# Performance work log

Hardware: AMD Instinct MI355X
Metric: run time of the kernel (lower is better)

The kernel has to match this reference:

```python
import jax, jax.numpy as jnp
import numpy as np

HIDDEN = 512
HEADS = 8
HEAD_DIM = HIDDEN // HEADS   # 64
MAN_DIM = 256                # manifold_dim = hidden_dim // 2
SCALE = HEAD_DIM ** -0.5


def _c(re, im):
    return jax.lax.complex(re, im)


def setup_inputs() -> dict:
    key = jax.random.key(0)
    ks = jax.random.split(key, 13)
    def w(k, shape, fan_in):
        return (jax.random.normal(k, shape, dtype=jnp.float32) / np.sqrt(fan_in)).astype(jnp.float32)
    B, S = 2, 2048
    return {
        "x": jax.random.normal(ks[0], (B, S, HIDDEN), dtype=jnp.float32),
        "Wq_re": w(ks[1], (HIDDEN, HIDDEN), HIDDEN), "Wq_im": w(ks[2], (HIDDEN, HIDDEN), HIDDEN),
        "Wk_re": w(ks[3], (HIDDEN, HIDDEN), HIDDEN), "Wk_im": w(ks[4], (HIDDEN, HIDDEN), HIDDEN),
        "Wv_re": w(ks[5], (HIDDEN, HIDDEN), HIDDEN), "Wv_im": w(ks[6], (HIDDEN, HIDDEN), HIDDEN),
        "Wm_re": w(ks[7], (HEAD_DIM, MAN_DIM), HEAD_DIM), "Wm_im": w(ks[8], (HEAD_DIM, MAN_DIM), HEAD_DIM),
        "Wmi_re": w(ks[9], (MAN_DIM, HEAD_DIM), MAN_DIM), "Wmi_im": w(ks[10], (MAN_DIM, HEAD_DIM), MAN_DIM),
        "Wo_re": w(ks[11], (HIDDEN, HIDDEN), HIDDEN), "Wo_im": w(ks[12], (HIDDEN, HIDDEN), HIDDEN),
    }


def reference(x, Wq_re, Wq_im, Wk_re, Wk_im, Wv_re, Wv_im,
              Wm_re, Wm_im, Wmi_re, Wmi_im, Wo_re, Wo_im):
    B, S, D = x.shape
    # quantum state preparation: cast to complex, L2-normalize along last dim
    xc = x.astype(jnp.complex64)
    norm = jnp.linalg.norm(xc, axis=-1, keepdims=True)
    xc = xc / norm

    Wq, Wk, Wv = _c(Wq_re, Wq_im), _c(Wk_re, Wk_im), _c(Wv_re, Wv_im)
    Wm, Wmi, Wo = _c(Wm_re, Wm_im), _c(Wmi_re, Wmi_im), _c(Wo_re, Wo_im)

    def heads(t):  # [B,S,D] -> [B,H,S,head_dim]
        return t.reshape(B, S, HEADS, HEAD_DIM).transpose(0, 2, 1, 3)

    q = heads(xc @ Wq)
    k = heads(xc @ Wk)
    v = heads(xc @ Wv)

    # project each head onto the manifold (complex linear)
    qm = jnp.einsum('bhsd,dm->bhsm', q, Wm)
    km = jnp.einsum('bhsd,dm->bhsm', k, Wm)
    vm = jnp.einsum('bhsd,dm->bhsm', v, Wm)

    # Hermitian inner product attention scores; softmax over real part
    scores = jnp.einsum('bhqm,bhkm->bhqk', qm, jnp.conj(km)) * SCALE
    attn = jax.nn.softmax(scores.real, axis=-1).astype(jnp.complex64)

    outm = jnp.einsum('bhqk,bhkm->bhqm', attn, vm)
    out = jnp.einsum('bhsm,md->bhsd', outm, Wmi)        # back to head_dim
    out = out.transpose(0, 2, 1, 3).reshape(B, S, D)    # merge heads
    out = out @ Wo
    # return real/imag stacked as float32 (complex64 output -> [B,S,D,2])
    return jnp.stack([out.real, out.imag], axis=-1)
```

## Files before the change

kernel.cpp:

```cpp
#include <hip/hip_runtime.h>
#include <hip/hip_bf16.h>
#include <stdint.h>


typedef __attribute__((ext_vector_type(8))) short bf16x8;
typedef __attribute__((ext_vector_type(4))) float f32x4;

#define QSCALE 0.18033688011112042f

__device__ __forceinline__ unsigned short f2b(float f) {
    union { float f; unsigned int u; } v; v.f = f;
    unsigned int r = v.u + 0x7fffu + ((v.u >> 16) & 1u);
    return (unsigned short)(r >> 16);
}

__device__ __forceinline__ unsigned int cvtpk(float a, float b) {
    union { __hip_bfloat162 h; unsigned int u; } v;
    v.h = __float22bfloat162_rn(make_float2(a, b));
    return v.u;
}

__device__ __forceinline__ void ld16(void* lds, const void* g) {
    __builtin_amdgcn_global_load_lds(
        (__attribute__((address_space(1))) unsigned int*)(g),
        (__attribute__((address_space(3))) unsigned int*)(lds), 16, 0, 0);
}

__global__ __launch_bounds__(256) void k_prep(
        const float* __restrict__ x, unsigned short* __restrict__ xn,
        const float* __restrict__ s0, const float* __restrict__ s1,
        const float* __restrict__ s2, const float* __restrict__ s3,
        const float* __restrict__ s4, const float* __restrict__ s5,
        const float* __restrict__ s6, const float* __restrict__ s7,
        float* __restrict__ d0, float* __restrict__ d1,
        float* __restrict__ d2, float* __restrict__ d3,
        float* __restrict__ d4, float* __restrict__ d5,
        float* __restrict__ d6, float* __restrict__ d7) {
    __shared__ float tile[64][65];
    if (blockIdx.x < 1024) {
        int row  = blockIdx.x * 4 + (threadIdx.x >> 6);
        int lane = threadIdx.x & 63;
        const float4* xr = (const float4*)(x + (size_t)row * 512);
        float4 a = xr[lane], b = xr[lane + 64];
        float s = a.x*a.x + a.y*a.y + a.z*a.z + a.w*a.w
                + b.x*b.x + b.y*b.y + b.z*b.z + b.w*b.w;
        #pragma unroll
        for (int m = 1; m < 64; m <<= 1) s += __shfl_xor(s, m, 64);
        float inv = 1.0f / sqrtf(s);
        ushort4 o;
        o.x = f2b(a.x*inv); o.y = f2b(a.y*inv); o.z = f2b(a.z*inv); o.w = f2b(a.w*inv);
        *(ushort4*)&xn[(size_t)row*512 + lane*4] = o;
        o.x = f2b(b.x*inv); o.y = f2b(b.y*inv); o.z = f2b(b.z*inv); o.w = f2b(b.w*inv);
        *(ushort4*)&xn[(size_t)row*512 + 256 + lane*4] = o;
        return;
    }
    int bid = blockIdx.x - 1024;
    const float* src; float* dst; int R, C, tr, tc;
    if (bid < 384) {
        int mat = bid >> 6, tl = bid & 63;
        src = (mat==0)?s0:(mat==1)?s1:(mat==2)?s2:(mat==3)?s3:(mat==4)?s4:s5;
        dst = (mat==0)?d0:(mat==1)?d1:(mat==2)?d2:(mat==3)?d3:(mat==4)?d4:d5;
        R = 512; C = 512; tr = tl >> 3; tc = tl & 7;
    } else {
        int mat = (bid - 384) >> 2, tl = (bid - 384) & 3;
        src = mat ? s7 : s6; dst = mat ? d7 : d6;
        R = 64; C = 256; tr = 0; tc = tl;
    }
    int r0 = tr * 64, c0 = tc * 64;
    int tx = threadIdx.x & 63, ty = threadIdx.x >> 6;
    #pragma unroll
    for (int i = 0; i < 16; i++) {
        int r = ty + i*4;
        tile[r][tx] = src[(size_t)(r0 + r)*C + c0 + tx];
    }
    __syncthreads();
    #pragma unroll
    for (int i = 0; i < 16; i++) {
        int r = ty + i*4;
        dst[(size_t)(c0 + r)*R + r0 + tx] = tile[tx][r];
    }
}

__global__ __launch_bounds__(256) void k_gh(const float* __restrict__ Wm_re, const float* __restrict__ Wm_im,
                                            const float* __restrict__ WmT_re, const float* __restrict__ WmT_im,
                                            const float* __restrict__ Wmi_re, const float* __restrict__ Wmi_im,
                                            float* __restrict__ GH) {
    int id = blockIdx.x * 256 + threadIdx.x;
    int mat = id >> 12;
    int a = (id >> 6) & 63, c = id & 63;
    float s = 0.f;
    if (mat < 2) {
        for (int m = 0; m < 256; m++) {
            float ar = Wm_re[a*256+m], ai = Wm_im[a*256+m];
            float br = WmT_re[m*64+c], bi = WmT_im[m*64+c];
            s += (mat == 0) ? (ar*br + ai*bi) : (ai*br - ar*bi);
        }
        GH[id] = s;
    } else {
        for (int m = 0; m < 256; m++) {
            float ar = Wm_re[a*256+m], ai = Wm_im[a*256+m];
            float br = Wmi_re[m*64+c], bi = Wmi_im[m*64+c];
            s += (mat == 2) ? (ar*br - ai*bi) : (ar*bi + ai*br);
        }
        GH[mat*4096 + c*64 + a] = s;
    }
}

__global__ __launch_bounds__(256) void k_pack(
        const float* __restrict__ WqT_re, const float* __restrict__ WqT_im,
        const float* __restrict__ WkT_re, const float* __restrict__ WkT_im,
        const float* __restrict__ WvT_re, const float* __restrict__ WvT_im,
        const float* __restrict__ Wo_re,  const float* __restrict__ Wo_im,
        const float* __restrict__ GH,
        unsigned short* __restrict__ WqkvT, unsigned short* __restrict__ Wbig) {
    if (blockIdx.x < 6144) {
        int id = blockIdx.x * 256 + threadIdx.x;
        int n = id >> 9, k = id & 511;
        float val;
        if (n < 1024) {
            int h = n >> 7, part = (n >> 6) & 1, j = n & 63;
            const float* Gr = GH;
            const float* Gi = GH + 4096;
            const float* qr = WqT_re + (size_t)(h*64)*512 + k;
            const float* qi = WqT_im + (size_t)(h*64)*512 + k;
            float s = 0.f;
            if (part == 0) { for (int d = 0; d < 64; d++) s += qr[d*512]*Gr[d*64+j] - qi[d*512]*Gi[d*64+j]; }
            else           { for (int d = 0; d < 64; d++) s += qr[d*512]*Gi[d*64+j] + qi[d*512]*Gr[d*64+j]; }
            val = s * QSCALE;
        } else if (n < 2048) {
            int m = n - 1024; int h = m >> 7, part = (m >> 6) & 1, j = m & 63;
            val = (part ? WkT_im : WkT_re)[(size_t)(h*64+j)*512 + k];
        } else {
            int m = n - 2048; int h = m >> 7, part = (m >> 6) & 1, j = m & 63;
            val = (part ? WvT_im : WvT_re)[(size_t)(h*64+j)*512 + k];
        }
        WqkvT[id] = f2b(val);
    } else {
        int id = (blockIdx.x - 6144) * 256 + threadIdx.x;
        int np = id >> 10, kk = id & 1023;
        int c = np >> 1, p = np & 1;
        int h = kk >> 7, pp = (kk >> 6) & 1, d = kk & 63;
        const float* HrT = GH + 2*4096;
        const float* HiT = GH + 3*4096;
        float s = 0.f;
        if (p == pp) {
            for (int j = 0; j < 64; j++) {
                float hr = HrT[j*64+d], hi = HiT[j*64+d];
                float wr = Wo_re[(size_t)(h*64+j)*512 + c];
                float wi = Wo_im[(size_t)(h*64+j)*512 + c];
                s += hr*wr - hi*wi;
            }
        } else {
            for (int j = 0; j < 64; j++) {
                float hr = HrT[j*64+d], hi = HiT[j*64+d];
                float wr = Wo_re[(size_t)(h*64+j)*512 + c];
                float wi = Wo_im[(size_t)(h*64+j)*512 + c];
                s += hr*wi + hi*wr;
            }
            if (p == 0) s = -s;
        }
        Wbig[(size_t)np*1024 + kk] = f2b(s);
    }
}

template<int MODE, int MT>
__global__ __launch_bounds__(256, 2) void k_gemm(
        const unsigned short* __restrict__ Ain, const unsigned short* __restrict__ Btin,
        void* __restrict__ Cout, unsigned short* __restrict__ Vt, int K) {
    __shared__ __align__(16) unsigned short Al[MT*32];
    __shared__ __align__(16) unsigned short Bl[128*32];
    const int t = threadIdx.x;
    const int wave = t >> 6, lane = t & 63, quad = lane >> 4, l16 = lane & 15;
    const int wr = wave >> 1, wc = wave & 1;

    const unsigned short* A;
    const unsigned short* Bt;
    unsigned short* Cb = nullptr;
    int m0, n0;
    if (MODE == 0) {
        if (blockIdx.y < 16) {
            A = Ain; Bt = Btin;
            m0 = blockIdx.x * 128; n0 = blockIdx.y * 128;
            Cb = (unsigned short*)Cout;
        } else {
            int idx = (blockIdx.y - 16) * 32 + blockIdx.x;
            int b = idx >> 7, mt = (idx >> 4) & 7, nt = idx & 15;
            A  = Btin + 2048*512;
            Bt = Ain + (size_t)b*2048*512;
            m0 = mt * 128; n0 = nt * 128;
            Cb = Vt + (size_t)b*1024*2048;
        }
    } else {
        A = Ain; Bt = Btin;
        m0 = blockIdx.x * MT; n0 = blockIdx.y * 128;
    }

    f32x4 acc[MT/32][4] = {};
    for (int kt = 0; kt < K; kt += 32) {
        #pragma unroll
        for (int i = 0; i < MT/64; i++) {
            int g = t + i*256, r = g >> 2, gr = g & 3;
            ld16(&Al[g*8], &A[(size_t)(m0 + r)*K + kt + gr*8]);
        }
        #pragma unroll
        for (int i = 0; i < 2; i++) {
            int g = t + i*256, r = g >> 2, gr = g & 3;
            ld16(&Bl[g*8], &Bt[(size_t)(n0 + r)*K + kt + gr*8]);
        }
        __syncthreads();
        bf16x8 af[MT/32], bfr[4];
        #pragma unroll
        for (int rt = 0; rt < MT/32; rt++)
            af[rt] = *(const bf16x8*)&Al[(wr*(MT/2) + rt*16 + l16)*32 + quad*8];
        #pragma unroll
        for (int ct = 0; ct < 4; ct++)
            bfr[ct] = *(const bf16x8*)&Bl[(wc*64 + ct*16 + l16)*32 + quad*8];
        #pragma unroll
        for (int rt = 0; rt < MT/32; rt++)
            #pragma unroll
            for (int ct = 0; ct < 4; ct++)
                acc[rt][ct] = __builtin_amdgcn_mfma_f32_16x16x32_bf16(af[rt], bfr[ct], acc[rt][ct], 0, 0, 0);
        __syncthreads();
    }
    #pragma unroll
    for (int rt = 0; rt < MT/32; rt++) {
        int row = m0 + wr*(MT/2) + rt*16 + quad*4;
        #pragma unroll
        for (int ct = 0; ct < 4; ct++) {
            int col = n0 + wc*64 + ct*16 + l16;
            if (MODE == 0) {
                unsigned int u01 = cvtpk(acc[rt][ct][0], acc[rt][ct][1]);
                unsigned int u23 = cvtpk(acc[rt][ct][2], acc[rt][ct][3]);
                Cb[(size_t)(row+0)*2048 + col] = (unsigned short)(u01);
                Cb[(size_t)(row+1)*2048 + col] = (unsigned short)(u01 >> 16);
                Cb[(size_t)(row+2)*2048 + col] = (unsigned short)(u23);
                Cb[(size_t)(row+3)*2048 + col] = (unsigned short)(u23 >> 16);
            } else {
                float* C = (float*)Cout;
                #pragma unroll
                for (int r = 0; r < 4; r++)
                    C[(size_t)(row + r)*1024 + col] = acc[rt][ct][r];
            }
        }
    }
}

__global__ __launch_bounds__(256, 2) void k_attn(
        const unsigned short* __restrict__ QK,
        const unsigned short* __restrict__ Vt,
        float* __restrict__ Opart,
        float* __restrict__ Lpart) {
    __shared__ __align__(16) unsigned short Kl[2][8192];
    __shared__ __align__(16) unsigned short Vl[2][8192];
    __shared__ __align__(16) unsigned short Pl[4608];

    const int t = threadIdx.x, w = t >> 6, lane = t & 63, quad = lane >> 4, l16 = lane & 15;
    const int bh = blockIdx.x, b = bh >> 3, h = bh & 7;
    const int qb = blockIdx.y & 15, half = blockIdx.y >> 4;
    const int tok0 = b*2048 + qb*128;

    bf16x8 qf[2][4];
    #pragma unroll
    for (int rt = 0; rt < 2; rt++)
        #pragma unroll
        for (int ks = 0; ks < 4; ks++)
            qf[rt][ks] = *(const bf16x8*)&QK[(size_t)(tok0 + w*32 + rt*16 + l16)*2048 + h*128 + ks*32 + quad*8];

    const unsigned short* kp = QK + (size_t)(b*2048 + half*1024 + (t >> 2))*2048 + 1024 + h*128 + (t & 3)*8;
    const unsigned short* vp = Vt + (size_t)(b*1024 + h*128 + (t >> 2))*2048 + half*1024 + (t & 3)*8;

    f32x4 Oacc[2][8] = {};
    float ls[2][4] = {};

    #pragma unroll
    for (int i = 0; i < 4; i++) ld16(&Kl[0][(i*256 + t)*8], kp + i*32);
    #pragma unroll
    for (int i = 0; i < 4; i++) ld16(&Vl[0][(i*256 + t)*8], vp + (i & 1)*131072 + (i >> 1)*32);
    __syncthreads();

    for (int it = 0; it < 16; it++) {
        const int cur = it & 1;
        if (it < 15) {
            int kt2 = (it + 1) * 64;
            #pragma unroll
            for (int i = 0; i < 4; i++) ld16(&Kl[cur^1][(i*256 + t)*8], kp + (size_t)kt2*2048 + i*32);
            #pragma unroll
            for (int i = 0; i < 4; i++) ld16(&Vl[cur^1][(i*256 + t)*8], vp + kt2 + (i & 1)*131072 + (i >> 1)*32);
        }

        f32x4 S[2][4] = {};
        #pragma unroll
        for (int ks = 0; ks < 4; ks++) {
            #pragma unroll
            for (int ct = 0; ct < 4; ct++) {
                bf16x8 kf = *(const bf16x8*)&Kl[cur][ks*2048 + (ct*16 + l16)*32 + quad*8];
                #pragma unroll
                for (int rt = 0; rt < 2; rt++)
                    S[rt][ct] = __builtin_amdgcn_mfma_f32_16x16x32_bf16(qf[rt][ks], kf, S[rt][ct], 0, 0, 0);
            }
        }
        #pragma unroll
        for (int ks2 = 0; ks2 < 2; ks2++) {
            #pragma unroll
            for (int rt = 0; rt < 2; rt++) {
                #pragma unroll
                for (int ct2 = 0; ct2 < 2; ct2++) {
                    int ct = ks2*2 + ct2;
                    float p0 = exp2f(S[rt][ct][0]), p1 = exp2f(S[rt][ct][1]);
                    float p2 = exp2f(S[rt][ct][2]), p3 = exp2f(S[rt][ct][3]);
                    ls[rt][0] += p0; ls[rt][1] += p1; ls[rt][2] += p2; ls[rt][3] += p3;
                    int q = w*32 + rt*16 + quad*4;
                    int base = ct2*16 + l16;
                    unsigned int u01 = cvtpk(p0, p1);
                    unsigned int u23 = cvtpk(p2, p3);
                    Pl[base + (q+0)*36] = (unsigned short)(u01);
                    Pl[base + (q+1)*36] = (unsigned short)(u01 >> 16);
                    Pl[base + (q+2)*36] = (unsigned short)(u23);
                    Pl[base + (q+3)*36] = (unsigned short)(u23 >> 16);
                }
            }
            bf16x8 pf[2];
            #pragma unroll
            for (int rt = 0; rt < 2; rt++)
                pf[rt] = *(const bf16x8*)&Pl[(w*32 + rt*16 + l16)*36 + quad*8];
            #pragma unroll
            for (int dt = 0; dt < 8; dt++) {
                bf16x8 vf = *(const bf16x8*)&Vl[cur][ks2*4096 + (dt*16 + l16)*32 + quad*8];
                #pragma unroll
                for (int rt = 0; rt < 2; rt++)
                    Oacc[rt][dt] = __builtin_amdgcn_mfma_f32_16x16x32_bf16(pf[rt], vf, Oacc[rt][dt], 0, 0, 0);
            }
        }
        __syncthreads();
    }

    #pragma unroll
    for (int rt = 0; rt < 2; rt++)
        #pragma unroll
        for (int r = 0; r < 4; r++) {
            float s = ls[rt][r];
            #pragma unroll
            for (int m = 1; m < 16; m <<= 1) s += __shfl_xor(s, m, 64);
            ls[rt][r] = s;
        }
    float* Op = Opart + (size_t)half*4096*1024;
    float* Lp = Lpart + (size_t)half*32768;
    #pragma unroll
    for (int rt = 0; rt < 2; rt++) {
        int q = w*32 + rt*16 + quad*4;
        int tok = tok0 + q;
        if (l16 == 0) {
            #pragma unroll
            for (int r = 0; r < 4; r++) Lp[(size_t)(tok + r)*8 + h] = ls[rt][r];
        }
        #pragma unroll
        for (int dt = 0; dt < 8; dt++) {
            int col = h*128 + dt*16 + l16;
            #pragma unroll
            for (int r = 0; r < 4; r++)
                Op[(size_t)(tok + r)*1024 + col] = Oacc[rt][dt][r];
        }
    }
}

__global__ __launch_bounds__(256) void k_merge(const float* __restrict__ Opart,
                                               const float* __restrict__ Lpart,
                                               unsigned short* __restrict__ O) {
    int tid = blockIdx.x * 256 + threadIdx.x;
    #pragma unroll
    for (int rep = 0; rep < 2; rep++) {
        int slot = tid + rep * 524288;
        int tok = slot >> 8, cg = slot & 255, h = cg >> 5;
        float l0 = Lpart[(size_t)tok*8 + h];
        float l1 = Lpart[32768 + (size_t)tok*8 + h];
        float inv = 1.0f / (l0 + l1);
        float4 a = ((const float4*)Opart)[slot];
        float4 b = ((const float4*)Opart)[1048576 + slot];
        unsigned int u01 = cvtpk((a.x + b.x)*inv, (a.y + b.y)*inv);
        unsigned int u23 = cvtpk((a.z + b.z)*inv, (a.w + b.w)*inv);
        ushort4 o;
        o.x = (unsigned short)u01; o.y = (unsigned short)(u01 >> 16);
        o.z = (unsigned short)u23; o.w = (unsigned short)(u23 >> 16);
        ((ushort4*)O)[slot] = o;
    }
}

extern "C" void kernel_launch(void* const* d_in, const int* in_sizes, int n_in,
                              void* d_out, int out_size, void* d_ws, size_t ws_size,
                              hipStream_t stream) {
    (void)in_sizes; (void)n_in; (void)out_size; (void)ws_size;
    const float* x      = (const float*)d_in[0];
    const float* Wq_re  = (const float*)d_in[1];
    const float* Wq_im  = (const float*)d_in[2];
    const float* Wk_re  = (const float*)d_in[3];
    const float* Wk_im  = (const float*)d_in[4];
    const float* Wv_re  = (const float*)d_in[5];
    const float* Wv_im  = (const float*)d_in[6];
    const float* Wm_re  = (const float*)d_in[7];
    const float* Wm_im  = (const float*)d_in[8];
    const float* Wmi_re = (const float*)d_in[9];
    const float* Wmi_im = (const float*)d_in[10];
    const float* Wo_re  = (const float*)d_in[11];
    const float* Wo_im  = (const float*)d_in[12];

    char* ws = (char*)d_ws;
    unsigned short* xn    = (unsigned short*)(ws);
    unsigned short* WqkvT = (unsigned short*)(ws + (4u << 20));
    unsigned short* Wbig  = (unsigned short*)(ws + (7u << 20));
    float*          GH    = (float*)         (ws + (9u << 20));
    float*          WmT_re= (float*)         (ws + (9u << 20) + (64u << 10));
    float*          WmT_im= (float*)         (ws + (9u << 20) + (128u << 10));
    unsigned short* QK    = (unsigned short*)(ws + (10u << 20));
    unsigned short* Vt    = (unsigned short*)(ws + (26u << 20));
    unsigned short* Obuf  = (unsigned short*)(ws + (34u << 20));
    float*          Opart = (float*)         (ws + (42u << 20));
    float*          Lpart = (float*)         (ws + (74u << 20));
    float* WqT_re = (float*)(ws + (10u << 20));
    float* WqT_im = (float*)(ws + (11u << 20));
    float* WkT_re = (float*)(ws + (12u << 20));
    float* WkT_im = (float*)(ws + (13u << 20));
    float* WvT_re = (float*)(ws + (14u << 20));
    float* WvT_im = (float*)(ws + (15u << 20));

    k_prep      <<<dim3(1416), dim3(256), 0, stream>>>(
        x, xn,
        Wq_re, Wq_im, Wk_re, Wk_im, Wv_re, Wv_im, Wm_re, Wm_im,
        WqT_re, WqT_im, WkT_re, WkT_im, WvT_re, WvT_im, WmT_re, WmT_im);
    k_gh        <<<dim3(64),   dim3(256), 0, stream>>>(Wm_re, Wm_im, WmT_re, WmT_im, Wmi_re, Wmi_im, GH);
    k_pack      <<<dim3(10240),dim3(256), 0, stream>>>(
        WqT_re, WqT_im, WkT_re, WkT_im, WvT_re, WvT_im, Wo_re, Wo_im, GH, WqkvT, Wbig);
    k_gemm<0,128><<<dim3(32, 24), dim3(256), 0, stream>>>(xn, WqkvT, (void*)QK, Vt, 512);
    k_attn      <<<dim3(16, 32), dim3(256), 0, stream>>>(QK, Vt, Opart, Lpart);
    k_merge     <<<dim3(2048), dim3(256), 0, stream>>>(Opart, Lpart, Obuf);
    k_gemm<1,64> <<<dim3(64, 8), dim3(256), 0, stream>>>(Obuf, Wbig, d_out, nullptr, 1024);
}
```

Measured before the change: 253.5 us.

## Split attention keys four ways with bf16 normalized partials and smaller tiles

The attention kernel now splits the key range into four quarters instead of two, doubling the grid to 1024 blocks. It uses 32-key tiles, so LDS per block is halved, and occupancy is raised to 3 blocks per CU. Each split normalizes its own output and stores it as bf16 rather than fp32, which cuts partial-buffer traffic. The merge kernel reads four bf16 partials and combines them with softmax-sum weights using vectorized loads. The trade-offs are extra bf16 rounding in the partials and more per-tile sync overhead.

```diff
diff --git a/kernel.cpp b/kernel.cpp
--- a/kernel.cpp
+++ b/kernel.cpp
@@ -12,6 +12,12 @@
     union { float f; unsigned int u; } v; v.f = f;
     unsigned int r = v.u + 0x7fffu + ((v.u >> 16) & 1u);
     return (unsigned short)(r >> 16);
+}
+
+__device__ __forceinline__ float b2f(short s) {
+    union { float f; unsigned int u; } v;
+    v.u = ((unsigned int)(unsigned short)s) << 16;
+    return v.f;
 }
 
 __device__ __forceinline__ unsigned int cvtpk(float a, float b) {
@@ -245,19 +251,20 @@
     }
 }
 
-__global__ __launch_bounds__(256, 2) void k_attn(
+__global__ __launch_bounds__(256, 3) void k_attn(
         const unsigned short* __restrict__ QK,
         const unsigned short* __restrict__ Vt,
-        float* __restrict__ Opart,
+        unsigned short* __restrict__ Opart,
         float* __restrict__ Lpart) {
-    __shared__ __align__(16) unsigned short Kl[2][8192];
-    __shared__ __align__(16) unsigned short Vl[2][8192];
+    __shared__ __align__(16) unsigned short Kl[2][4096];
+    __shared__ __align__(16) unsigned short Vl[2][4096];
     __shared__ __align__(16) unsigned short Pl[4608];
 
     const int t = threadIdx.x, w = t >> 6, lane = t & 63, quad = lane >> 4, l16 = lane & 15;
     const int bh = blockIdx.x, b = bh >> 3, h = bh & 7;
-    const int qb = blockIdx.y & 15, half = blockIdx.y >> 4;
+    const int qb = blockIdx.y >> 2, quarter = blockIdx.y & 3;
     const int tok0 = b*2048 + qb*128;
+    const int key0 = quarter*512;
 
     bf16x8 qf[2][4];
     #pragma unroll
@@ -266,70 +273,67 @@
         for (int ks = 0; ks < 4; ks++)
             qf[rt][ks] = *(const bf16x8*)&QK[(size_t)(tok0 + w*32 + rt*16 + l16)*2048 + h*128 + ks*32 + quad*8];
 
-    const unsigned short* kp = QK + (size_t)(b*2048 + half*1024 + (t >> 2))*2048 + 1024 + h*128 + (t & 3)*8;
-    const unsigned short* vp = Vt + (size_t)(b*1024 + h*128 + (t >> 2))*2048 + half*1024 + (t & 3)*8;
+    const unsigned short* kp = QK + (size_t)(b*2048 + key0 + ((t >> 2) & 31))*2048 + 1024 + h*128
+                               + (t >> 7)*32 + (t & 3)*8;
+    const unsigned short* vp = Vt + (size_t)(b*1024 + h*128 + (t >> 2))*2048 + key0 + (t & 3)*8;
 
     f32x4 Oacc[2][8] = {};
     float ls[2][4] = {};
 
     #pragma unroll
-    for (int i = 0; i < 4; i++) ld16(&Kl[0][(i*256 + t)*8], kp + i*32);
-    #pragma unroll
-    for (int i = 0; i < 4; i++) ld16(&Vl[0][(i*256 + t)*8], vp + (i & 1)*131072 + (i >> 1)*32);
+    for (int i = 0; i < 2; i++) ld16(&Kl[0][(i*256 + t)*8], kp + i*64);
+    #pragma unroll
+    for (int i = 0; i < 2; i++) ld16(&Vl[0][(i*256 + t)*8], vp + (size_t)i*64*2048);
     __syncthreads();
 
     for (int it = 0; it < 16; it++) {
         const int cur = it & 1;
         if (it < 15) {
-            int kt2 = (it + 1) * 64;
-            #pragma unroll
-            for (int i = 0; i < 4; i++) ld16(&Kl[cur^1][(i*256 + t)*8], kp + (size_t)kt2*2048 + i*32);
-            #pragma unroll
-            for (int i = 0; i < 4; i++) ld16(&Vl[cur^1][(i*256 + t)*8], vp + kt2 + (i & 1)*131072 + (i >> 1)*32);
-        }
-
-        f32x4 S[2][4] = {};
+            int kt2 = (it + 1) * 32;
+            #pragma unroll
+            for (int i = 0; i < 2; i++) ld16(&Kl[cur^1][(i*256 + t)*8], kp + (size_t)kt2*2048 + i*64);
+            #pragma unroll
+            for (int i = 0; i < 2; i++) ld16(&Vl[cur^1][(i*256 + t)*8], vp + kt2 + (size_t)i*64*2048);
+        }
+
+        f32x4 S[2][2] = {};
         #pragma unroll
         for (int ks = 0; ks < 4; ks++) {
             #pragma unroll
-            for (int ct = 0; ct < 4; ct++) {
-                bf16x8 kf = *(const bf16x8*)&Kl[cur][ks*2048 + (ct*16 + l16)*32 + quad*8];
+            for (int ct = 0; ct < 2; ct++) {
+                bf16x8 kf = *(const bf16x8*)&Kl[cur][ks*1024 + (ct*16 + l16)*32 + quad*8];
                 #pragma unroll
                 for (int rt = 0; rt < 2; rt++)
                     S[rt][ct] = __builtin_amdgcn_mfma_f32_16x16x32_bf16(qf[rt][ks], kf, S[rt][ct], 0, 0, 0);
             }
         }
         #pragma unroll
-        for (int ks2 = 0; ks2 < 2; ks2++) {
-            #pragma unroll
-            for (int rt = 0; rt < 2; rt++) {
-                #pragma unroll
-                for (int ct2 = 0; ct2 < 2; ct2++) {
-                    int ct = ks2*2 + ct2;
-                    float p0 = exp2f(S[rt][ct][0]), p1 = exp2f(S[rt][ct][1]);
-                    float p2 = exp2f(S[rt][ct][2]), p3 = exp2f(S[rt][ct][3]);
-                    ls[rt][0] += p0; ls[rt][1] += p1; ls[rt][2] += p2; ls[rt][3] += p3;
-                    int q = w*32 + rt*16 + quad*4;
-                    int base = ct2*16 + l16;
-                    unsigned int u01 = cvtpk(p0, p1);
-                    unsigned int u23 = cvtpk(p2, p3);
-                    Pl[base + (q+0)*36] = (unsigned short)(u01);
-                    Pl[base + (q+1)*36] = (unsigned short)(u01 >> 16);
-                    Pl[base + (q+2)*36] = (unsigned short)(u23);
-                    Pl[base + (q+3)*36] = (unsigned short)(u23 >> 16);
-                }
+        for (int rt = 0; rt < 2; rt++) {
+            #pragma unroll
+            for (int ct = 0; ct < 2; ct++) {
+                float p0 = exp2f(S[rt][ct][0]), p1 = exp2f(S[rt][ct][1]);
+                float p2 = exp2f(S[rt][ct][2]), p3 = exp2f(S[rt][ct][3]);
+                ls[rt][0] += p0; ls[rt][1] += p1; ls[rt][2] += p2; ls[rt][3] += p3;
+                int q = w*32 + rt*16 + quad*4;
+                int base = ct*16 + l16;
+                unsigned int u01 = cvtpk(p0, p1);
+                unsigned int u23 = cvtpk(p2, p3);
+                Pl[base + (q+0)*36] = (unsigned short)(u01);
+                Pl[base + (q+1)*36] = (unsigned short)(u01 >> 16);
+                Pl[base + (q+2)*36] = (unsigned short)(u23);
+                Pl[base + (q+3)*36] = (unsigned short)(u23 >> 16);
             }
-            bf16x8 pf[2];
+        }
+        bf16x8 pf[2];
+        #pragma unroll
+        for (int rt = 0; rt < 2; rt++)
+            pf[rt] = *(const bf16x8*)&Pl[(w*32 + rt*16 + l16)*36 + quad*8];
+        #pragma unroll
+        for (int dt = 0; dt < 8; dt++) {
+            bf16x8 vf = *(const bf16x8*)&Vl[cur][(dt*16 + l16)*32 + quad*8];
             #pragma unroll
             for (int rt = 0; rt < 2; rt++)
-                pf[rt] = *(const bf16x8*)&Pl[(w*32 + rt*16 + l16)*36 + quad*8];
-            #pragma unroll
-            for (int dt = 0; dt < 8; dt++) {
-                bf16x8 vf = *(const bf16x8*)&Vl[cur][ks2*4096 + (dt*16 + l16)*32 + quad*8];
-                #pragma unroll
-                for (int rt = 0; rt < 2; rt++)
-                    Oacc[rt][dt] = __builtin_amdgcn_mfma_f32_16x16x32_bf16(pf[rt], vf, Oacc[rt][dt], 0, 0, 0);
-            }
+                Oacc[rt][dt] = __builtin_amdgcn_mfma_f32_16x16x32_bf16(pf[rt], vf, Oacc[rt][dt], 0, 0, 0);
         }
         __syncthreads();
     }
@@ -343,12 +347,15 @@
             for (int m = 1; m < 16; m <<= 1) s += __shfl_xor(s, m, 64);
             ls[rt][r] = s;
         }
-    float* Op = Opart + (size_t)half*4096*1024;
-    float* Lp = Lpart + (size_t)half*32768;
+    unsigned short* Op = Opart + (size_t)quarter*4096*1024;
+    float* Lp = Lpart + (size_t)quarter*32768;
     #pragma unroll
     for (int rt = 0; rt < 2; rt++) {
         int q = w*32 + rt*16 + quad*4;
         int tok = tok0 + q;
+        float inv[4];
+        #pragma unroll
+        for (int r = 0; r < 4; r++) inv[r] = 1.0f / ls[rt][r];
         if (l16 == 0) {
             #pragma unroll
             for (int r = 0; r < 4; r++) Lp[(size_t)(tok + r)*8 + h] = ls[rt][r];
@@ -358,31 +365,35 @@
             int col = h*128 + dt*16 + l16;
             #pragma unroll
             for (int r = 0; r < 4; r++)
-                Op[(size_t)(tok + r)*1024 + col] = Oacc[rt][dt][r];
-        }
-    }
-}
-
-__global__ __launch_bounds__(256) void k_merge(const float* __restrict__ Opart,
+                Op[(size_t)(tok + r)*1024 + col] = f2b(Oacc[rt][dt][r] * inv[r]);
+        }
+    }
+}
+
+__global__ __launch_bounds__(256) void k_merge(const unsigned short* __restrict__ Opart,
                                                const float* __restrict__ Lpart,
                                                unsigned short* __restrict__ O) {
-    int tid = blockIdx.x * 256 + threadIdx.x;
-    #pragma unroll
-    for (int rep = 0; rep < 2; rep++) {
-        int slot = tid + rep * 524288;
-        int tok = slot >> 8, cg = slot & 255, h = cg >> 5;
-        float l0 = Lpart[(size_t)tok*8 + h];
-        float l1 = Lpart[32768 + (size_t)tok*8 + h];
-        float inv = 1.0f / (l0 + l1);
-        float4 a = ((const float4*)Opart)[slot];
-        float4 b = ((const float4*)Opart)[1048576 + slot];
-        unsigned int u01 = cvtpk((a.x + b.x)*inv, (a.y + b.y)*inv);
-        unsigned int u23 = cvtpk((a.z + b.z)*inv, (a.w + b.w)*inv);
-        ushort4 o;
-        o.x = (unsigned short)u01; o.y = (unsigned short)(u01 >> 16);
-        o.z = (unsigned short)u23; o.w = (unsigned short)(u23 >> 16);
-        ((ushort4*)O)[slot] = o;
-    }
+    int slot = blockIdx.x * 256 + threadIdx.x;
+    int tok = slot >> 7, colg = slot & 127, h = colg >> 4;
+    float l0 = Lpart[(size_t)tok*8 + h];
+    float l1 = Lpart[32768 + (size_t)tok*8 + h];
+    float l2 = Lpart[65536 + (size_t)tok*8 + h];
+    float l3 = Lpart[98304 + (size_t)tok*8 + h];
+    float inv = 1.0f / (l0 + l1 + l2 + l3);
+    float w0 = l0*inv, w1 = l1*inv, w2 = l2*inv, w3 = l3*inv;
+    size_t off = (size_t)tok*1024 + colg*8;
+    bf16x8 a0 = *(const bf16x8*)&Opart[off];
+    bf16x8 a1 = *(const bf16x8*)&Opart[4194304 + off];
+    bf16x8 a2 = *(const bf16x8*)&Opart[8388608 + off];
+    bf16x8 a3 = *(const bf16x8*)&Opart[12582912 + off];
+    float o[8];
+    #pragma unroll
+    for (int j = 0; j < 8; j++)
+        o[j] = w0*b2f(a0[j]) + w1*b2f(a1[j]) + w2*b2f(a2[j]) + w3*b2f(a3[j]);
+    uint4 uo;
+    uo.x = cvtpk(o[0], o[1]); uo.y = cvtpk(o[2], o[3]);
+    uo.z = cvtpk(o[4], o[5]); uo.w = cvtpk(o[6], o[7]);
+    *(uint4*)&O[off] = uo;
 }
 
 extern "C" void kernel_launch(void* const* d_in, const int* in_sizes, int n_in,
@@ -413,7 +424,7 @@
     unsigned short* QK    = (unsigned short*)(ws + (10u << 20));
     unsigned short* Vt    = (unsigned short*)(ws + (26u << 20));
     unsigned short* Obuf  = (unsigned short*)(ws + (34u << 20));
-    float*          Opart = (float*)         (ws + (42u << 20));
+    unsigned short* Opart = (unsigned short*)(ws + (42u << 20));
     float*          Lpart = (float*)         (ws + (74u << 20));
     float* WqT_re = (float*)(ws + (10u << 20));
     float* WqT_im = (float*)(ws + (11u << 20));
@@ -430,7 +441,7 @@
     k_pack      <<<dim3(10240),dim3(256), 0, stream>>>(
         WqT_re, WqT_im, WkT_re, WkT_im, WvT_re, WvT_im, Wo_re, Wo_im, GH, WqkvT, Wbig);
     k_gemm<0,128><<<dim3(32, 24), dim3(256), 0, stream>>>(xn, WqkvT, (void*)QK, Vt, 512);
-    k_attn      <<<dim3(16, 32), dim3(256), 0, stream>>>(QK, Vt, Opart, Lpart);
+    k_attn      <<<dim3(16, 64), dim3(256), 0, stream>>>(QK, Vt, Opart, Lpart);
     k_merge     <<<dim3(2048), dim3(256), 0, stream>>>(Opart, Lpart, Obuf);
     k_gemm<1,64> <<<dim3(64, 8), dim3(256), 0, stream>>>(Obuf, Wbig, d_out, nullptr, 1024);
 }
```

Result: slower. 260.5 us (+2.8%).

## Fuse split-KV merge into output GEMM and store partial attention outputs in bf16

Applied to the files above, without the earlier changes.

The attention kernel now normalises each half's partial output by its own softmax sum and writes it as bf16 instead of fp32. The separate merge kernel is removed. The output GEMM combines the two halves on the fly while loading its A tile, weighting each half by its share of the total sum. The GEMM K-loop also now processes 64 per iteration over two LDS stages, halving the barriers. Together these remove a kernel launch and the fp32 write/read round trip. The cost is redundant merge work in the GEMM A-load (each A tile is re-merged for all 8 column blocks) and a synchronous register-path load instead of direct-to-LDS for MODE 1.

```diff
diff --git a/kernel.cpp b/kernel.cpp
--- a/kernel.cpp
+++ b/kernel.cpp
@@ -12,6 +12,12 @@
     union { float f; unsigned int u; } v; v.f = f;
     unsigned int r = v.u + 0x7fffu + ((v.u >> 16) & 1u);
     return (unsigned short)(r >> 16);
+}
+
+__device__ __forceinline__ float b2f(short s) {
+    union { float f; unsigned int u; } v;
+    v.u = ((unsigned int)(unsigned short)s) << 16;
+    return v.f;
 }
 
 __device__ __forceinline__ unsigned int cvtpk(float a, float b) {
@@ -166,9 +172,10 @@
 template<int MODE, int MT>
 __global__ __launch_bounds__(256, 2) void k_gemm(
         const unsigned short* __restrict__ Ain, const unsigned short* __restrict__ Btin,
-        void* __restrict__ Cout, unsigned short* __restrict__ Vt, int K) {
-    __shared__ __align__(16) unsigned short Al[MT*32];
-    __shared__ __align__(16) unsigned short Bl[128*32];
+        void* __restrict__ Cout, unsigned short* __restrict__ Vt,
+        const float* __restrict__ Lp, int K) {
+    __shared__ __align__(16) unsigned short Al[2][MT*32];
+    __shared__ __align__(16) unsigned short Bl[2][128*32];
     const int t = threadIdx.x;
     const int wave = t >> 6, lane = t & 63, quad = lane >> 4, l16 = lane & 15;
     const int wr = wave >> 1, wc = wave & 1;
@@ -196,30 +203,60 @@
     }
 
     f32x4 acc[MT/32][4] = {};
-    for (int kt = 0; kt < K; kt += 32) {
-        #pragma unroll
-        for (int i = 0; i < MT/64; i++) {
-            int g = t + i*256, r = g >> 2, gr = g & 3;
-            ld16(&Al[g*8], &A[(size_t)(m0 + r)*K + kt + gr*8]);
-        }
-        #pragma unroll
-        for (int i = 0; i < 2; i++) {
-            int g = t + i*256, r = g >> 2, gr = g & 3;
-            ld16(&Bl[g*8], &Bt[(size_t)(n0 + r)*K + kt + gr*8]);
-        }
+    for (int kt = 0; kt < K; kt += 64) {
+        if (MODE == 1) {
+            int r = t >> 2, gr = t & 3;
+            int row = m0 + r;
+            #pragma unroll
+            for (int kh = 0; kh < 2; kh++) {
+                int kk = kt + kh*32 + gr*8;
+                int hh = kk >> 7;
+                float l0 = Lp[(size_t)row*8 + hh];
+                float l1 = Lp[32768 + (size_t)row*8 + hh];
+                float invl = 1.0f / (l0 + l1);
+                float w0 = l0*invl, w1 = l1*invl;
+                size_t off = (size_t)row*1024 + kk;
+                bf16x8 a0 = *(const bf16x8*)&Ain[off];
+                bf16x8 a1 = *(const bf16x8*)&Ain[4194304 + off];
+                uint4 u;
+                u.x = cvtpk(w0*b2f(a0[0]) + w1*b2f(a1[0]), w0*b2f(a0[1]) + w1*b2f(a1[1]));
+                u.y = cvtpk(w0*b2f(a0[2]) + w1*b2f(a1[2]), w0*b2f(a0[3]) + w1*b2f(a1[3]));
+                u.z = cvtpk(w0*b2f(a0[4]) + w1*b2f(a1[4]), w0*b2f(a0[5]) + w1*b2f(a1[5]));
+                u.w = cvtpk(w0*b2f(a0[6]) + w1*b2f(a1[6]), w0*b2f(a0[7]) + w1*b2f(a1[7]));
+                *(uint4*)&Al[kh][t*8] = u;
+            }
+        } else {
+            #pragma unroll
+            for (int kh = 0; kh < 2; kh++)
+                #pragma unroll
+                for (int i = 0; i < MT/64; i++) {
+                    int g = t + i*256, r = g >> 2, gr = g & 3;
+                    ld16(&Al[kh][g*8], &A[(size_t)(m0 + r)*K + kt + kh*32 + gr*8]);
+                }
+        }
+        #pragma unroll
+        for (int kh = 0; kh < 2; kh++)
+            #pragma unroll
+            for (int i = 0; i < 2; i++) {
+                int g = t + i*256, r = g >> 2, gr = g & 3;
+                ld16(&Bl[kh][g*8], &Bt[(size_t)(n0 + r)*K + kt + kh*32 + gr*8]);
+            }
         __syncthreads();
-        bf16x8 af[MT/32], bfr[4];
-        #pragma unroll
-        for (int rt = 0; rt < MT/32; rt++)
-            af[rt] = *(const bf16x8*)&Al[(wr*(MT/2) + rt*16 + l16)*32 + quad*8];
-        #pragma unroll
-        for (int ct = 0; ct < 4; ct++)
-            bfr[ct] = *(const bf16x8*)&Bl[(wc*64 + ct*16 + l16)*32 + quad*8];
-        #pragma unroll
-        for (int rt = 0; rt < MT/32; rt++)
+        #pragma unroll
+        for (int kh = 0; kh < 2; kh++) {
+            bf16x8 af[MT/32], bfr[4];
+            #pragma unroll
+            for (int rt = 0; rt < MT/32; rt++)
+                af[rt] = *(const bf16x8*)&Al[kh][(wr*(MT/2) + rt*16 + l16)*32 + quad*8];
             #pragma unroll
             for (int ct = 0; ct < 4; ct++)
-                acc[rt][ct] = __builtin_amdgcn_mfma_f32_16x16x32_bf16(af[rt], bfr[ct], acc[rt][ct], 0, 0, 0);
+                bfr[ct] = *(const bf16x8*)&Bl[kh][(wc*64 + ct*16 + l16)*32 + quad*8];
+            #pragma unroll
+            for (int rt = 0; rt < MT/32; rt++)
+                #pragma unroll
+                for (int ct = 0; ct < 4; ct++)
+                    acc[rt][ct] = __builtin_amdgcn_mfma_f32_16x16x32_bf16(af[rt], bfr[ct], acc[rt][ct], 0, 0, 0);
+        }
         __syncthreads();
     }
     #pragma unroll
@@ -248,7 +285,7 @@
 __global__ __launch_bounds__(256, 2) void k_attn(
         const unsigned short* __restrict__ QK,
         const unsigned short* __restrict__ Vt,
-        float* __restrict__ Opart,
+        unsigned short* __restrict__ Opart,
         float* __restrict__ Lpart) {
     __shared__ __align__(16) unsigned short Kl[2][8192];
     __shared__ __align__(16) unsigned short Vl[2][8192];
@@ -343,12 +380,15 @@
             for (int m = 1; m < 16; m <<= 1) s += __shfl_xor(s, m, 64);
             ls[rt][r] = s;
         }
-    float* Op = Opart + (size_t)half*4096*1024;
+    unsigned short* Op = Opart + (size_t)half*4096*1024;
     float* Lp = Lpart + (size_t)half*32768;
     #pragma unroll
     for (int rt = 0; rt < 2; rt++) {
         int q = w*32 + rt*16 + quad*4;
         int tok = tok0 + q;
+        float inv[4];
+        #pragma unroll
+        for (int r = 0; r < 4; r++) inv[r] = 1.0f / ls[rt][r];
         if (l16 == 0) {
             #pragma unroll
             for (int r = 0; r < 4; r++) Lp[(size_t)(tok + r)*8 + h] = ls[rt][r];
@@ -358,30 +398,8 @@
             int col = h*128 + dt*16 + l16;
             #pragma unroll
             for (int r = 0; r < 4; r++)
-                Op[(size_t)(tok + r)*1024 + col] = Oacc[rt][dt][r];
-        }
-    }
-}
-
-__global__ __launch_bounds__(256) void k_merge(const float* __restrict__ Opart,
-                                               const float* __restrict__ Lpart,
-                                               unsigned short* __restrict__ O) {
-    int tid = blockIdx.x * 256 + threadIdx.x;
-    #pragma unroll
-    for (int rep = 0; rep < 2; rep++) {
-        int slot = tid + rep * 524288;
-        int tok = slot >> 8, cg = slot & 255, h = cg >> 5;
-        float l0 = Lpart[(size_t)tok*8 + h];
-        float l1 = Lpart[32768 + (size_t)tok*8 + h];
-        float inv = 1.0f / (l0 + l1);
-        float4 a = ((const float4*)Opart)[slot];
-        float4 b = ((const float4*)Opart)[1048576 + slot];
-        unsigned int u01 = cvtpk((a.x + b.x)*inv, (a.y + b.y)*inv);
-        unsigned int u23 = cvtpk((a.z + b.z)*inv, (a.w + b.w)*inv);
-        ushort4 o;
-        o.x = (unsigned short)u01; o.y = (unsigned short)(u01 >> 16);
-        o.z = (unsigned short)u23; o.w = (unsigned short)(u23 >> 16);
-        ((ushort4*)O)[slot] = o;
+                Op[(size_t)(tok + r)*1024 + col] = f2b(Oacc[rt][dt][r] * inv[r]);
+        }
     }
 }
 
@@ -412,8 +430,7 @@
     float*          WmT_im= (float*)         (ws + (9u << 20) + (128u << 10));
     unsigned short* QK    = (unsigned short*)(ws + (10u << 20));
     unsigned short* Vt    = (unsigned short*)(ws + (26u << 20));
-    unsigned short* Obuf  = (unsigned short*)(ws + (34u << 20));
-    float*          Opart = (float*)         (ws + (42u << 20));
+    unsigned short* Opart = (unsigned short*)(ws + (42u << 20));
     float*          Lpart = (float*)         (ws + (74u << 20));
     float* WqT_re = (float*)(ws + (10u << 20));
     float* WqT_im = (float*)(ws + (11u << 20));
@@ -429,8 +446,7 @@
     k_gh        <<<dim3(64),   dim3(256), 0, stream>>>(Wm_re, Wm_im, WmT_re, WmT_im, Wmi_re, Wmi_im, GH);
     k_pack      <<<dim3(10240),dim3(256), 0, stream>>>(
         WqT_re, WqT_im, WkT_re, WkT_im, WvT_re, WvT_im, Wo_re, Wo_im, GH, WqkvT, Wbig);
-    k_gemm<0,128><<<dim3(32, 24), dim3(256), 0, stream>>>(xn, WqkvT, (void*)QK, Vt, 512);
+    k_gemm<0,128><<<dim3(32, 24), dim3(256), 0, stream>>>(xn, WqkvT, (void*)QK, Vt, nullptr, 512);
     k_attn      <<<dim3(16, 32), dim3(256), 0, stream>>>(QK, Vt, Opart, Lpart);
-    k_merge     <<<dim3(2048), dim3(256), 0, stream>>>(Opart, Lpart, Obuf);
-    k_gemm<1,64> <<<dim3(64, 8), dim3(256), 0, stream>>>(Obuf, Wbig, d_out, nullptr, 1024);
-}
+    k_gemm<1,64> <<<dim3(64, 8), dim3(256), 0, stream>>>(Opart, Wbig, d_out, nullptr, Lpart, 1024);
+}
```

Result: faster. 246.0 us (-2.9%).
